# Performance work log

Measured on AMD Instinct MI355X. Metric: run time of the kernel, lower is better.

The kernel has to match this reference:

```python
import jax, jax.numpy as jnp
import numpy as np

MAX_DEPTH = 8          # inner-node depths 1..8; leaves at depth 9
LMBDA = 0.1            # args.lmbda; per-node lmbda = LMBDA * 2**(-depth)
EPS = 1e-6


def setup_inputs() -> dict:
    key = jax.random.key(0)
    ks = jax.random.split(key, 7)
    B, D, O = 16384, 2048, 1000
    n_inner = 2 ** MAX_DEPTH - 1   # 255
    n_leaf = 2 ** MAX_DEPTH       # 256
    x = jax.random.normal(ks[0], (B, D), dtype=jnp.float32)
    target = jax.random.randint(ks[1], (B,), 0, O)
    y = jax.nn.one_hot(target, O, dtype=jnp.float32)  # target_onehot
    W = jax.random.normal(ks[2], (n_inner, D), dtype=jnp.float32) / np.sqrt(D)
    b = jax.random.normal(ks[3], (n_inner,), dtype=jnp.float32) * 0.01
    beta = jax.random.normal(ks[4], (n_inner,), dtype=jnp.float32)
    leaf_params = jax.random.normal(ks[5], (n_leaf, O), dtype=jnp.float32)
    return {"x": x, "y": y, "W": W, "b": b, "beta": beta, "leaf_params": leaf_params}


def reference(x, y, W, b, beta, leaf_params):
    """Faithful vectorized version of SoftDecisionTree.cal_loss.
    Inner nodes are stored in level-order (heap) layout, left-to-right
    within each level, matching the left-first recursion of cal_prob.
    Returns (loss, output) like cal_loss.
    """
    B = x.shape[0]
    dt = x.dtype
    # All inner-node gates in one fused GEMM: sigmoid(beta * (x @ w + b))
    probs = jax.nn.sigmoid(beta * (x @ W.T + b))  # [B, n_inner]

    path = jnp.ones((B, 1), dt)  # path_prob_init
    C = jnp.asarray(0.0, dt)
    idx = 0
    for d in range(1, MAX_DEPTH + 1):  # small fixed loop over tree levels
        n = 2 ** (d - 1)
        p = probs[:, idx:idx + n]      # gate probs for this level's nodes [B, n]
        if d < MAX_DEPTH:              # get_penalty skips nodes whose children are leaves
            denom = jnp.sum(path, axis=0)                  # [n]
            denom = jnp.where(denom == 0, EPS, denom)
            alpha = jnp.sum(p * path, axis=0) / denom      # [n]
            alpha = jnp.clip(alpha, EPS, 1.0 - EPS)
            lmbda = LMBDA * 2.0 ** (-d)
            C = C - jnp.sum(lmbda * 0.5 * (jnp.log(alpha) + jnp.log1p(-alpha)))
        # children: left gets path*(1-p), right gets path*p, interleaved
        path = jnp.stack([path * (1.0 - p), path * p], axis=-1).reshape(B, 2 * n)
        idx += n
    # path: [B, n_leaf] leaf arrival probabilities (left-to-right leaf order)

    logQ = jax.nn.log_softmax(leaf_params, axis=-1)  # [n_leaf, O]
    TQ = y @ logQ.T                                  # [B, n_leaf]: y . log Q per leaf
    loss_term = jnp.mean(jnp.sum(path * TQ, axis=1))
    loss = -loss_term + C

    best = jnp.argmax(path, axis=1)   # first max, matches the '<' update order
    output = jnp.exp(logQ)[best]      # [B, O] max_Q
    return loss, output
```

## Files before the change

kernel.cpp:

```cpp
#include <hip/hip_runtime.h>


typedef __attribute__((ext_vector_type(8))) short short8;
typedef __attribute__((ext_vector_type(4))) float f32x4;

#define DIM 2048
#define NCLS 1000
#define NINNER 255
#define NPAD 256
#define PSTRIDE (16384ull * NPAD)

__device__ __forceinline__ unsigned cvt2bf(float a, float b) {
  return ((__float_as_uint(a) + 0x8000u) >> 16) | ((__float_as_uint(b) + 0x8000u) & 0xFFFF0000u);
}

__device__ __forceinline__ void async_copy16(const unsigned short* gsrc, unsigned short* ldst) {
  __builtin_amdgcn_global_load_lds(
      (const __attribute__((address_space(1))) unsigned int*)(gsrc),
      (__attribute__((address_space(3))) unsigned int*)(ldst), 16, 0, 0);
}

__global__ __launch_bounds__(256) void prep_w(const float* __restrict__ W,
                                              const float* __restrict__ b,
                                              const float* __restrict__ beta,
                                              unsigned short* __restrict__ Wb,
                                              float* __restrict__ bp,
                                              float* __restrict__ betap) {
  int i = blockIdx.x * 256 + threadIdx.x;
  int n = i >> 11;
  float v = (n < NINNER) ? W[i] : 0.f;
  Wb[i] = (unsigned short)((__float_as_uint(v) + 0x8000u) >> 16);
  if (i < NPAD) {
    bp[i] = (i < NINNER) ? b[i] : 0.f;
    betap[i] = (i < NINNER) ? beta[i] : 0.f;
  }
}

__global__ __launch_bounds__(256) void leaf_softmax(const float* __restrict__ leaf,
                                                    float* __restrict__ logQT,
                                                    float* __restrict__ Q) {
  int l = blockIdx.x, t = threadIdx.x;
  const float* row = leaf + (size_t)l * NCLS;
  __shared__ float red[256];
  float mx = -3.4e38f;
  for (int j = t; j < NCLS; j += 256) mx = fmaxf(mx, row[j]);
  red[t] = mx; __syncthreads();
  for (int s = 128; s; s >>= 1) { if (t < s) red[t] = fmaxf(red[t], red[t + s]); __syncthreads(); }
  mx = red[0]; __syncthreads();
  float sm = 0.f;
  for (int j = t; j < NCLS; j += 256) sm += __expf(row[j] - mx);
  red[t] = sm; __syncthreads();
  for (int s = 128; s; s >>= 1) { if (t < s) red[t] += red[t + s]; __syncthreads(); }
  float lse = mx + __logf(red[0]);
  for (int j = t; j < NCLS; j += 256) {
    float lg = row[j] - lse;
    logQT[(size_t)j * NPAD + l] = lg;
    Q[(size_t)l * NCLS + j] = __expf(lg);
  }
}

__global__ __launch_bounds__(256) void find_targets(const float* __restrict__ y,
                                                    int* __restrict__ tgt) {
  int wv = threadIdx.x >> 6, lane = threadIdx.x & 63;
  int r = blockIdx.x * 4 + wv;
  const float4* yr = (const float4*)(y + (size_t)r * NCLS);
  int found = 0x7fffffff;
#pragma unroll
  for (int i = 0; i < 4; ++i) {
    int j4 = i * 64 + lane;
    if (j4 < 250) {
      float4 v = yr[j4];
      if (v.x > 0.5f) found = min(found, 4 * j4 + 0);
      if (v.y > 0.5f) found = min(found, 4 * j4 + 1);
      if (v.z > 0.5f) found = min(found, 4 * j4 + 2);
      if (v.w > 0.5f) found = min(found, 4 * j4 + 3);
    }
  }
  for (int off = 32; off; off >>= 1) found = min(found, __shfl_down(found, off));
  if (lane == 0) tgt[r] = found;
}

__global__ __launch_bounds__(256, 4) void gemm_xwT(const float* __restrict__ x,
                                                   const unsigned short* __restrict__ Wb,
                                                   float* __restrict__ P) {
  __shared__ __align__(16) unsigned short As[64 * 40];
  __shared__ __align__(16) unsigned short Bs[256 * 32];

  int tid = threadIdx.x;
  int lane = tid & 63, wave = tid >> 6;
  int m_base = blockIdx.x * 64;
  int k_base = blockIdx.z * 512;
  float* Pz = P + (size_t)blockIdx.z * PSTRIDE;

  f32x4 acc[4][4] = {};

  int arow = tid >> 2, aseg = tid & 3;
  const float* aptr = x + (size_t)(m_base + arow) * DIM + k_base + aseg * 8;
  unsigned short* asd = &As[arow * 40 + aseg * 8];

  int rr = lane >> 2;
  int sg = (lane & 3) ^ ((rr + (rr >> 2)) & 3);
  const unsigned short* bg0 = Wb + (size_t)(wave * 64 + rr) * DIM + k_base + sg * 8;
  const unsigned short* bg1 = bg0 + 16 * DIM;
  const unsigned short* bg2 = bg0 + 32 * DIM;
  const unsigned short* bg3 = bg0 + 48 * DIM;
  unsigned short* bl0 = &Bs[(wave * 4 + 0) * 512];
  unsigned short* bl1 = &Bs[(wave * 4 + 1) * 512];
  unsigned short* bl2 = &Bs[(wave * 4 + 2) * 512];
  unsigned short* bl3 = &Bs[(wave * 4 + 3) * 512];

  int frow = lane & 15, q = lane >> 4;
  int bseg = (q ^ ((frow + (frow >> 2)) & 3)) * 8;
  int wcol = wave * 64;

  for (int kt = 0; kt < 512; kt += 32) {
    float4 v0 = *(const float4*)(aptr + kt);
    float4 v1 = *(const float4*)(aptr + kt + 4);
    uint4 pk;
    pk.x = cvt2bf(v0.x, v0.y); pk.y = cvt2bf(v0.z, v0.w);
    pk.z = cvt2bf(v1.x, v1.y); pk.w = cvt2bf(v1.z, v1.w);
    __syncthreads();
    *(uint4*)asd = pk;
    async_copy16(bg0 + kt, bl0);
    async_copy16(bg1 + kt, bl1);
    async_copy16(bg2 + kt, bl2);
    async_copy16(bg3 + kt, bl3);
    __syncthreads();
    short8 a[4];
#pragma unroll
    for (int mt = 0; mt < 4; ++mt)
      a[mt] = *(const short8*)&As[(mt * 16 + frow) * 40 + q * 8];
#pragma unroll
    for (int nt = 0; nt < 4; ++nt) {
      short8 bb = *(const short8*)&Bs[(wcol + nt * 16 + frow) * 32 + bseg];
#pragma unroll
      for (int mt = 0; mt < 4; ++mt)
        acc[mt][nt] = __builtin_amdgcn_mfma_f32_16x16x32_bf16(a[mt], bb, acc[mt][nt], 0, 0, 0);
    }
  }
#pragma unroll
  for (int mt = 0; mt < 4; ++mt) {
#pragma unroll
    for (int rg = 0; rg < 4; ++rg) {
      float* dst = Pz + (size_t)(m_base + mt * 16 + q * 4 + rg) * NPAD + wcol + frow;
#pragma unroll
      for (int nt = 0; nt < 4; ++nt) dst[nt * 16] = acc[mt][nt][rg];
    }
  }
}

__global__ __launch_bounds__(256) void tree_walk(const float* __restrict__ P,
                                                 const float* __restrict__ bp,
                                                 const float* __restrict__ betap,
                                                 const float* __restrict__ logQT,
                                                 const int* __restrict__ tgt,
                                                 float* __restrict__ acc,
                                                 int* __restrict__ best) {
  __shared__ float ws[4][256];
  __shared__ float s0s[127], s1s[127];
  __shared__ float sdot;
  int tid = threadIdx.x;
  int lane = tid & 63, wv = tid >> 6;
  if (tid < 127) { s0s[tid] = 0.f; s1s[tid] = 0.f; }
  if (tid == 255) sdot = 0.f;
  __syncthreads();
  float4 bb = *(const float4*)(bp + lane * 4);
  float4 be = *(const float4*)(betap + lane * 4);
  float* wsp = ws[wv];
  float wdot = 0.f;
  for (int it = 0; it < 4; ++it) {
    int r = blockIdx.x * 16 + wv * 4 + it;
    const float* pr = P + (size_t)r * NPAD + lane * 4;
    float4 u0 = *(const float4*)(pr);
    float4 u1 = *(const float4*)(pr + PSTRIDE);
    float4 u2 = *(const float4*)(pr + 2 * PSTRIDE);
    float4 u3 = *(const float4*)(pr + 3 * PSTRIDE);
    float4 pz;
    pz.x = 1.f / (1.f + __expf(-be.x * (u0.x + u1.x + u2.x + u3.x + bb.x)));
    pz.y = 1.f / (1.f + __expf(-be.y * (u0.y + u1.y + u2.y + u3.y + bb.y)));
    pz.z = 1.f / (1.f + __expf(-be.z * (u0.z + u1.z + u2.z + u3.z + bb.z)));
    pz.w = 1.f / (1.f + __expf(-be.w * (u0.w + u1.w + u2.w + u3.w + bb.w)));
    *(float4*)(wsp + lane * 4) = pz;
    __asm__ volatile("" ::: "memory");
    int tg = tgt[r];
    float pp = 1.f;
#pragma unroll
    for (int d = 1; d <= 6; ++d) {
      int idx = (1 << (d - 1)) - 1 + (lane >> (7 - d));
      float p = wsp[idx];
      if ((lane & ((1 << (7 - d)) - 1)) == 0) {
        atomicAdd(&s0s[idx], pp);
        atomicAdd(&s1s[idx], p * pp);
      }
      pp *= ((lane >> (6 - d)) & 1) ? p : (1.f - p);
    }
    float p7 = wsp[63 + lane];
    atomicAdd(&s0s[63 + lane], pp);
    atomicAdd(&s1s[63 + lane], p7 * pp);
    float pL = pp * (1.f - p7), pR = pp * p7;
    float p8a = wsp[127 + 2 * lane], p8b = wsp[128 + 2 * lane];
    float lf0 = pL * (1.f - p8a), lf1 = pL * p8a;
    float lf2 = pR * (1.f - p8b), lf3 = pR * p8b;
    float4 lq = *(const float4*)(logQT + (size_t)tg * NPAD + lane * 4);
    wdot += lf0 * lq.x + lf1 * lq.y + lf2 * lq.z + lf3 * lq.w;
    float bv = lf0; int bi = 4 * lane;
    if (lf1 > bv) { bv = lf1; bi = 4 * lane + 1; }
    if (lf2 > bv) { bv = lf2; bi = 4 * lane + 2; }
    if (lf3 > bv) { bv = lf3; bi = 4 * lane + 3; }
    for (int off = 32; off; off >>= 1) {
      float ov = __shfl_down(bv, off);
      int oi = __shfl_down(bi, off);
      if (ov > bv || (ov == bv && oi < bi)) { bv = ov; bi = oi; }
    }
    if (lane == 0) best[r] = bi;
  }
  for (int off = 32; off; off >>= 1) wdot += __shfl_down(wdot, off);
  if (lane == 0) atomicAdd(&sdot, wdot);
  __syncthreads();
  if (tid < 127) {
    atomicAdd(&acc[tid], s0s[tid]);
    atomicAdd(&acc[127 + tid], s1s[tid]);
  }
  if (tid == 255) atomicAdd(&acc[254], sdot);
}

__global__ __launch_bounds__(128) void finalize_loss(const float* __restrict__ acc,
                                                     float* __restrict__ out) {
  __shared__ float red[128];
  int t = threadIdx.x;
  float c = 0.f;
  if (t < 127) {
    float denom = acc[t];
    if (denom == 0.f) denom = 1e-6f;
    float alpha = acc[127 + t] / denom;
    alpha = fminf(fmaxf(alpha, 1e-6f), 1.f - 1e-6f);
    int d = 31 - __clz(t + 1) + 1;
    float lm = 0.1f * exp2f(-(float)d);
    c = -lm * 0.5f * (logf(alpha) + log1pf(-alpha));
  }
  red[t] = c;
  __syncthreads();
  for (int s = 64; s; s >>= 1) { if (t < s) red[t] += red[t + s]; __syncthreads(); }
  if (t == 0) out[0] = -(acc[254] / 16384.f) + red[0];
}

__global__ __launch_bounds__(256) void gather_rows(const float* __restrict__ Q,
                                                   const int* __restrict__ best,
                                                   float* __restrict__ out) {
  int wv = threadIdx.x >> 6, lane = threadIdx.x & 63;
  int r = blockIdx.x * 4 + wv;
  const float* src = Q + (size_t)best[r] * NCLS;
  float* dst = out + 1 + (size_t)r * NCLS;
  if (lane < 3) dst[lane] = src[lane];
  if (lane == 0) dst[999] = src[999];
#pragma unroll
  for (int i = 0; i < 4; ++i) {
    int q = i * 64 + lane;
    if (q < 249) {
      int o = 3 + 4 * q;
      float4 v = make_float4(src[o], src[o + 1], src[o + 2], src[o + 3]);
      *(float4*)(dst + o) = v;
    }
  }
}

extern "C" void kernel_launch(void* const* d_in, const int* in_sizes, int n_in,
                              void* d_out, int out_size, void* d_ws, size_t ws_size,
                              hipStream_t stream) {
  const float* x = (const float*)d_in[0];
  const float* y = (const float*)d_in[1];
  const float* W = (const float*)d_in[2];
  const float* b = (const float*)d_in[3];
  const float* beta = (const float*)d_in[4];
  const float* leaf = (const float*)d_in[5];
  float* out = (float*)d_out;
  char* ws = (char*)d_ws;

  unsigned short* Wb = (unsigned short*)(ws + 0);
  float* bp    = (float*)(ws + 1048576);
  float* betap = (float*)(ws + 1049600);
  float* acc   = (float*)(ws + 1050624);
  int* tgt     = (int*)(ws + 1051648);
  int* best    = (int*)(ws + 1117184);
  float* logQT = (float*)(ws + 1182720);
  float* Q     = (float*)(ws + 2206720);
  float* P     = (float*)(ws + 3230720);

  prep_w<<<2048, 256, 0, stream>>>(W, b, beta, Wb, bp, betap);
  leaf_softmax<<<256, 256, 0, stream>>>(leaf, logQT, Q);
  find_targets<<<4096, 256, 0, stream>>>(y, tgt);
  gemm_xwT<<<dim3(256, 1, 4), 256, 0, stream>>>(x, Wb, P);
  hipMemsetAsync(acc, 0, 256 * sizeof(float), stream);
  tree_walk<<<1024, 256, 0, stream>>>(P, bp, betap, logQT, tgt, acc, best);
  finalize_loss<<<1, 128, 0, stream>>>(acc, out);
  gather_rows<<<4096, 256, 0, stream>>>(Q, best, out);
}
```

Baseline: 365.1 us.

## Stage whole A K-slice in swizzled LDS and drop per-step block barriers

```diff
diff --git a/kernel.cpp b/kernel.cpp
--- a/kernel.cpp
+++ b/kernel.cpp
@@ -80,10 +80,10 @@
   if (lane == 0) tgt[r] = found;
 }
 
-__global__ __launch_bounds__(256, 4) void gemm_xwT(const float* __restrict__ x,
+__global__ __launch_bounds__(256, 2) void gemm_xwT(const float* __restrict__ x,
                                                    const unsigned short* __restrict__ Wb,
                                                    float* __restrict__ P) {
-  __shared__ __align__(16) unsigned short As[64 * 40];
+  __shared__ __align__(16) unsigned short As[64 * 512];
   __shared__ __align__(16) unsigned short Bs[256 * 32];
 
   int tid = threadIdx.x;
@@ -91,12 +91,6 @@
   int m_base = blockIdx.x * 64;
   int k_base = blockIdx.z * 512;
   float* Pz = P + (size_t)blockIdx.z * PSTRIDE;
-
-  f32x4 acc[4][4] = {};
-
-  int arow = tid >> 2, aseg = tid & 3;
-  const float* aptr = x + (size_t)(m_base + arow) * DIM + k_base + aseg * 8;
-  unsigned short* asd = &As[arow * 40 + aseg * 8];
 
   int rr = lane >> 2;
   int sg = (lane & 3) ^ ((rr + (rr >> 2)) & 3);
@@ -108,36 +102,71 @@
   unsigned short* bl1 = &Bs[(wave * 4 + 1) * 512];
   unsigned short* bl2 = &Bs[(wave * 4 + 2) * 512];
   unsigned short* bl3 = &Bs[(wave * 4 + 3) * 512];
-
+  async_copy16(bg0, bl0);
+  async_copy16(bg1, bl1);
+  async_copy16(bg2, bl2);
+  async_copy16(bg3, bl3);
+
+  {
+    int r = tid >> 2, c = tid & 3;
+    const float* ap = x + (size_t)(m_base + r) * DIM + k_base + c * 128;
+    unsigned short* arow = &As[r * 512];
+    int xr = r & 7;
+#pragma unroll
+    for (int j = 0; j < 2; ++j) {
+      float4 f[16];
+#pragma unroll
+      for (int i = 0; i < 16; ++i) f[i] = *(const float4*)(ap + j * 64 + i * 4);
+#pragma unroll
+      for (int u = 0; u < 8; ++u) {
+        uint4 pk;
+        pk.x = cvt2bf(f[2 * u].x, f[2 * u].y);
+        pk.y = cvt2bf(f[2 * u].z, f[2 * u].w);
+        pk.z = cvt2bf(f[2 * u + 1].x, f[2 * u + 1].y);
+        pk.w = cvt2bf(f[2 * u + 1].z, f[2 * u + 1].w);
+        int s = c * 16 + j * 8 + u;
+        *(uint4*)&arow[(s ^ xr) * 8] = pk;
+      }
+    }
+  }
+  __syncthreads();
+
+  f32x4 acc[4][4] = {};
   int frow = lane & 15, q = lane >> 4;
   int bseg = (q ^ ((frow + (frow >> 2)) & 3)) * 8;
   int wcol = wave * 64;
-
-  for (int kt = 0; kt < 512; kt += 32) {
-    float4 v0 = *(const float4*)(aptr + kt);
-    float4 v1 = *(const float4*)(aptr + kt + 4);
-    uint4 pk;
-    pk.x = cvt2bf(v0.x, v0.y); pk.y = cvt2bf(v0.z, v0.w);
-    pk.z = cvt2bf(v1.x, v1.y); pk.w = cvt2bf(v1.z, v1.w);
-    __syncthreads();
-    *(uint4*)asd = pk;
-    async_copy16(bg0 + kt, bl0);
-    async_copy16(bg1 + kt, bl1);
-    async_copy16(bg2 + kt, bl2);
-    async_copy16(bg3 + kt, bl3);
-    __syncthreads();
-    short8 a[4];
+  int am[4], xm[4];
+#pragma unroll
+  for (int mt = 0; mt < 4; ++mt) {
+    int m = mt * 16 + frow;
+    am[mt] = m * 512;
+    xm[mt] = m & 7;
+  }
+
+  for (int kt = 0; kt < 16; ++kt) {
+    __asm__ volatile("s_waitcnt vmcnt(0)" ::: "memory");
+    short8 a[4], bb[4];
 #pragma unroll
     for (int mt = 0; mt < 4; ++mt)
-      a[mt] = *(const short8*)&As[(mt * 16 + frow) * 40 + q * 8];
-#pragma unroll
-    for (int nt = 0; nt < 4; ++nt) {
-      short8 bb = *(const short8*)&Bs[(wcol + nt * 16 + frow) * 32 + bseg];
+      a[mt] = *(const short8*)&As[am[mt] + (((kt * 4 + q) ^ xm[mt]) * 8)];
+#pragma unroll
+    for (int nt = 0; nt < 4; ++nt)
+      bb[nt] = *(const short8*)&Bs[(wcol + nt * 16 + frow) * 32 + bseg];
+    __asm__ volatile("s_waitcnt lgkmcnt(0)" ::: "memory");
+    if (kt < 15) {
+      int ko = (kt + 1) * 32;
+      async_copy16(bg0 + ko, bl0);
+      async_copy16(bg1 + ko, bl1);
+      async_copy16(bg2 + ko, bl2);
+      async_copy16(bg3 + ko, bl3);
+    }
+#pragma unroll
+    for (int nt = 0; nt < 4; ++nt)
 #pragma unroll
       for (int mt = 0; mt < 4; ++mt)
-        acc[mt][nt] = __builtin_amdgcn_mfma_f32_16x16x32_bf16(a[mt], bb, acc[mt][nt], 0, 0, 0);
-    }
-  }
+        acc[mt][nt] = __builtin_amdgcn_mfma_f32_16x16x32_bf16(a[mt], bb[nt], acc[mt][nt], 0, 0, 0);
+  }
+
 #pragma unroll
   for (int mt = 0; mt < 4; ++mt) {
 #pragma unroll
```

New measurement: 367.8 us. No clear change (+0.7%).
